# Kernel optimization log

Hardware: AMD Instinct MI355X
Metric: run time of the kernel (lower is better)

Reference implementation:

```python
import jax, jax.numpy as jnp
import numpy as np

V = 10000      # vocabulary_size
T = 20         # max_len
D = 512        # D_img == hidden size
H = 64         # actor/critic hidden
FI = 2048      # image feature dim
FB = 256       # box feature dim (FI + FB == 2304)
B = 1024       # batch
N_WORDS = 50   # allowed word_list size


def setup_inputs() -> dict:
    key = jax.random.key(0)
    ks = iter(jax.random.split(key, 40))
    def p(shape, s=0.02):
        return (jax.random.normal(next(ks), shape) * s).astype(jnp.float32)
    z = lambda *s: jnp.zeros(s, jnp.float32)
    inp = {
        "image_feature": jax.random.normal(next(ks), (B, FI), dtype=jnp.float32),
        "box_feature": jax.random.normal(next(ks), (B, FB), dtype=jnp.float32),
        # feature_resizer Linear(2304, D)
        "fr_w": p((FI + FB, D)), "fr_b": z(D),
        # _block dense1 / dense2 (each: Linear(D,D), GELU, Linear(D,D))
        "d1a_w": p((D, D)), "d1a_b": z(D), "d1b_w": p((D, D)), "d1b_b": z(D),
        "d2a_w": p((D, D)), "d2a_b": z(D), "d2b_w": p((D, D)), "d2b_b": z(D),
        # encoder LayerNorm (affine) + Linear(D, 512)
        "ln_g": jnp.ones((D,), jnp.float32), "ln_b": z(D),
        "eo_w": p((D, 512)), "eo_b": z(512),
        # word embedding
        "emb": p((V, 512)),
        # GRUCell weights, torch gate order (r, z, n)
        "gwi": p((512, 3 * 512)), "gwh": p((512, 3 * 512)),
        "gbi": z(3 * 512), "gbh": z(3 * 512),
        # actor: 512->64 tanh 64->64 tanh 64->V
        "a1_w": p((512, H)), "a1_b": z(H),
        "a2_w": p((H, H)), "a2_b": z(H),
        "a3_w": p((H, V), 0.01), "a3_b": z(V),
        # critic: 512->64 tanh 64->64 tanh 64->1
        "c1_w": p((512, H)), "c1_b": z(H),
        "c2_w": p((H, H)), "c2_b": z(H),
        "c3_w": p((H, 1)), "c3_b": z(1),
        # frozen word mask: 0 for allowed words, -1000 otherwise
        "word_mask": jnp.where(jnp.arange(V) < N_WORDS, 0.0, -1000.0).astype(jnp.float32),
    }
    return inp


def _ln(x, g=None, b=None):
    m = x.mean(-1, keepdims=True)
    v = x.var(-1, keepdims=True)
    y = (x - m) * jax.lax.rsqrt(v + 1e-5)
    return y if g is None else y * g + b


def _forward(image_feature, box_feature, fr_w, fr_b,
             d1a_w, d1a_b, d1b_w, d1b_b, d2a_w, d2a_b, d2b_w, d2b_b,
             ln_g, ln_b, eo_w, eo_b, emb, gwi, gwh, gbi, gbh,
             a1_w, a1_b, a2_w, a2_b, a3_w, a3_b,
             c1_w, c1_b, c2_w, c2_b, c3_w, c3_b, word_mask):
    gelu = lambda t: jax.nn.gelu(t, approximate=False)
    # feature resizer + residual block + LN + projection (encoder)
    x0 = jnp.concatenate([image_feature, box_feature], axis=1) @ fr_w + fr_b
    y = gelu(_ln(x0) @ d1a_w + d1a_b) @ d1b_w + d1b_b
    y = _ln(y + x0)
    x = x0 + (gelu(y @ d2a_w + d2a_b) @ d2b_w + d2b_b)
    img = _ln(x, ln_g, ln_b) @ eo_w + eo_b          # [B, 512]

    samp_key = jax.random.key(1)

    def step(carry, t):
        hx, ix = carry
        # torch: hx = GRUCell(input=hx, hidden=ix)
        gi = hx @ gwi + gbi
        gh = ix @ gwh + gbh
        gir, giz, gin = jnp.split(gi, 3, axis=-1)
        ghr, ghz, ghn = jnp.split(gh, 3, axis=-1)
        r = jax.nn.sigmoid(gir + ghr)
        zg = jax.nn.sigmoid(giz + ghz)
        n = jnp.tanh(gin + r * ghn)
        h = (1.0 - zg) * n + zg * ix                # new hidden [B, 512]
        logits = jnp.tanh(jnp.tanh(h @ a1_w + a1_b) @ a2_w + a2_b) @ a3_w + a3_b + word_mask
        logp = jax.nn.log_softmax(logits, axis=-1)  # [B, V]
        act = jax.random.categorical(jax.random.fold_in(samp_key, t), logp, axis=-1)  # [B]
        lp = jnp.take_along_axis(logp, act[:, None], axis=-1)[:, 0]
        ent = -jnp.sum(jnp.exp(logp) * logp, axis=-1)
        val = (jnp.tanh(jnp.tanh(h @ c1_w + c1_b) @ c2_w + c2_b) @ c3_w + c3_b)[:, 0]
        return (h, emb[act]), (act, lp, ent, val)

    _, (acts, lps, ents, vals) = jax.lax.scan(step, (img, jnp.zeros_like(img)), jnp.arange(T))
    # scan stacks along time first -> transpose to [B, T]
    return acts.T, lps.T, ents.T, vals.T[..., None]


def reference(image_feature, box_feature, fr_w, fr_b,
              d1a_w, d1a_b, d1b_w, d1b_b, d2a_w, d2a_b, d2b_w, d2b_b,
              ln_g, ln_b, eo_w, eo_b, emb, gwi, gwh, gbi, gbh,
              a1_w, a1_b, a2_w, a2_b, a3_w, a3_b,
              c1_w, c1_b, c2_w, c2_b, c3_w, c3_b, word_mask):
    return _forward(image_feature, box_feature, fr_w, fr_b,
                    d1a_w, d1a_b, d1b_w, d1b_b, d2a_w, d2a_b, d2b_w, d2b_b,
                    ln_g, ln_b, eo_w, eo_b, emb, gwi, gwh, gbi, gbh,
                    a1_w, a1_b, a2_w, a2_b, a3_w, a3_b,
                    c1_w, c1_b, c2_w, c2_b, c3_w, c3_b, word_mask)
```

## Files before the change

### kernel.cpp

```cpp
#include <hip/hip_runtime.h>
#include <math.h>
#include <stdint.h>

#define BB 1024
#define DD 512
#define VV 10000
#define TT 20
#define NW 50

__host__ __device__ __forceinline__ void tf2x32(uint32_t k0, uint32_t k1,
                                                uint32_t x0, uint32_t x1,
                                                uint32_t& o0, uint32_t& o1) {
  uint32_t ks2 = k0 ^ k1 ^ 0x1BD11BDAu;
  x0 += k0; x1 += k1;
#define ROTL(x,r) (((x)<<(r))|((x)>>(32-(r))))
#define RND(r) { x0 += x1; x1 = ROTL(x1,(r)); x1 ^= x0; }
  RND(13) RND(15) RND(26) RND(6)   x0 += k1;  x1 += ks2 + 1u;
  RND(17) RND(29) RND(16) RND(24)  x0 += ks2; x1 += k0 + 2u;
  RND(13) RND(15) RND(26) RND(6)   x0 += k0;  x1 += k1 + 3u;
  RND(17) RND(29) RND(16) RND(24)  x0 += k1;  x1 += ks2 + 4u;
  RND(13) RND(15) RND(26) RND(6)   x0 += ks2; x1 += k0 + 5u;
#undef RND
#undef ROTL
  o0 = x0; o1 = x1;
}

__device__ __forceinline__ float wave_sum(float v) {
#pragma unroll
  for (int o = 32; o > 0; o >>= 1) v += __shfl_xor(v, o, 64);
  return v;
}
__device__ __forceinline__ float wave_max(float v) {
#pragma unroll
  for (int o = 32; o > 0; o >>= 1) v = fmaxf(v, __shfl_xor(v, o, 64));
  return v;
}

__device__ __forceinline__ float gelu_f(float x) {
  float u = x / 1.4142135623730951f;
  float e = (float)erf((double)u);
  return x * (e + 1.0f) * 0.5f;
}

template<int MR, int ACT, bool RES, bool CONCAT>
__global__ __launch_bounds__(64) void wgemm_k(
    const float* __restrict__ A, const float* __restrict__ A2, int K1,
    const float* __restrict__ W, int ldw, const float* __restrict__ bias,
    const float* __restrict__ res, float* __restrict__ C, int N, int K)
{
  constexpr int TM = MR * 8;
  constexpr int ASTR = (TM == 64) ? 72 : 40;
  constexpr int WSTR = 40;
  constexpr int PA_N = (TM == 64) ? 16 : 8;
  __shared__ alignas(16) float As[64][ASTR];
  __shared__ alignas(16) float Ws[64][WSTR];
  const int bm = blockIdx.x * TM;
  const int bn = blockIdx.y * 32;
  const int lane = threadIdx.x;
  const int tr = (lane >> 3) * MR;
  const int tc = (lane & 7) << 2;
  const int arow = (TM == 64) ? lane : (lane & 31);
  const int akb  = (TM == 64) ? 0 : ((lane >> 5) * 32);
  const int wr0 = lane >> 3;
  const int wc  = (lane & 7) << 2;

  float4 pa[PA_N], pw[8];
  auto load_tile = [&](int k0) {
#pragma unroll
    for (int h = 0; h < PA_N; h++) {
      int gk = k0 + akb + 4 * h;
      if (CONCAT) {
        pa[h] = (gk < K1) ? *(const float4*)&A[(size_t)(bm + arow) * K1 + gk]
                          : *(const float4*)&A2[(size_t)(bm + arow) * (K - K1) + (gk - K1)];
      } else {
        pa[h] = *(const float4*)&A[(size_t)(bm + arow) * K + gk];
      }
    }
#pragma unroll
    for (int h = 0; h < 8; h++) {
      pw[h] = *(const float4*)&W[(size_t)(k0 + wr0 + 8 * h) * ldw + bn + wc];
    }
  };

  float acc[MR][4];
#pragma unroll
  for (int i = 0; i < MR; i++)
#pragma unroll
    for (int j = 0; j < 4; j++) acc[i][j] = 0.f;

  load_tile(0);
  for (int k0 = 0; k0 < K; k0 += 64) {
#pragma unroll
    for (int h = 0; h < PA_N; h++) {
      int kb = akb + 4 * h;
      As[kb + 0][arow] = pa[h].x; As[kb + 1][arow] = pa[h].y;
      As[kb + 2][arow] = pa[h].z; As[kb + 3][arow] = pa[h].w;
    }
#pragma unroll
    for (int h = 0; h < 8; h++) *(float4*)&Ws[wr0 + 8 * h][wc] = pw[h];
    if (k0 + 64 < K) load_tile(k0 + 64);
#pragma unroll
    for (int kk = 0; kk < 64; kk++) {
      float4 bv = *(const float4*)&Ws[kk][tc];
#pragma unroll
      for (int ih = 0; ih < MR / 4; ih++) {
        float4 av = *(const float4*)&As[kk][tr + 4 * ih];
        float* ap = (float*)&av;
#pragma unroll
        for (int q = 0; q < 4; q++) {
          int i = 4 * ih + q;
          acc[i][0] = fmaf(ap[q], bv.x, acc[i][0]);
          acc[i][1] = fmaf(ap[q], bv.y, acc[i][1]);
          acc[i][2] = fmaf(ap[q], bv.z, acc[i][2]);
          acc[i][3] = fmaf(ap[q], bv.w, acc[i][3]);
        }
      }
    }
  }
#pragma unroll
  for (int i = 0; i < MR; i++) {
    int m = bm + tr + i;
    float4 o;
    float* op = (float*)&o;
#pragma unroll
    for (int j = 0; j < 4; j++) {
      int n = bn + tc + j;
      float v = acc[i][j] + bias[n];
      if (ACT == 1) v = gelu_f(v);
      if (RES) v = v + res[(size_t)m * N + n];
      op[j] = v;
    }
    *(float4*)&C[(size_t)m * N + bn + tc] = o;
  }
}

template<bool AFFINE, bool ADD>
__global__ __launch_bounds__(256) void lnorm_k(
    const float* __restrict__ X, const float* __restrict__ X2,
    const float* __restrict__ g, const float* __restrict__ bt,
    float* __restrict__ Y)
{
  __shared__ float red[8];
  int row = blockIdx.x, tid = threadIdx.x;
  const float* x = X + (size_t)row * DD;
  float v0 = x[tid], v1 = x[tid + 256];
  if (ADD) {
    const float* x2 = X2 + (size_t)row * DD;
    v0 += x2[tid]; v1 += x2[tid + 256];
  }
  float s = wave_sum(v0 + v1);
  if ((tid & 63) == 0) red[tid >> 6] = s;
  __syncthreads();
  float mean = (red[0] + red[1] + red[2] + red[3]) * (1.0f / 512.0f);
  float d0 = v0 - mean, d1 = v1 - mean;
  float s2 = wave_sum(d0 * d0 + d1 * d1);
  if ((tid & 63) == 0) red[4 + (tid >> 6)] = s2;
  __syncthreads();
  float var = (red[4] + red[5] + red[6] + red[7]) * (1.0f / 512.0f);
  float rs = (float)(1.0 / sqrt((double)(var + 1e-5f)));
  float y0 = d0 * rs, y1 = d1 * rs;
  if (AFFINE) {
    y0 = y0 * g[tid] + bt[tid];
    y1 = y1 * g[tid + 256] + bt[tid + 256];
  }
  Y[(size_t)row * DD + tid] = y0;
  Y[(size_t)row * DD + tid + 256] = y1;
}

__global__ __launch_bounds__(256) void gru_head(
    const float* __restrict__ gi, const float* __restrict__ table,
    const float* __restrict__ gbh, const float* __restrict__ emb,
    const float* __restrict__ a1w, const float* __restrict__ a1b,
    const float* __restrict__ a2w, const float* __restrict__ a2b,
    const float* __restrict__ a3w, const float* __restrict__ a3b,
    const float* __restrict__ c1w, const float* __restrict__ c1b,
    const float* __restrict__ c2w, const float* __restrict__ c2b,
    const float* __restrict__ c3w, const float* __restrict__ c3b,
    const float* __restrict__ wmask,
    float* __restrict__ hx, float* __restrict__ out,
    int t, uint32_t fk0, uint32_t fk1)
{
  int w = threadIdx.x >> 6;
  int lane = threadIdx.x & 63;
  int b = blockIdx.x * 4 + w;
  __shared__ float sh[4][DD];
  __shared__ float st1[4][64], st2[4][64], sc1[4][64];

  int a = (t > 0) ? (int)out[(size_t)b * TT + (t - 1)] : -1;
  const float* ghb = (a >= 0) ? (table + (size_t)a * 1536) : gbh;
  const float* gib = gi + (size_t)b * 1536;
  const float* er  = (a >= 0) ? (emb + (size_t)a * DD) : nullptr;
#pragma unroll
  for (int jj = 0; jj < 8; jj++) {
    int j = lane + 64 * jj;
    float ixv = (a >= 0) ? er[j] : 0.f;
    float r = (float)(1.0 / (1.0 + exp(-(double)(gib[j] + ghb[j]))));
    float z = (float)(1.0 / (1.0 + exp(-(double)(gib[DD + j] + ghb[DD + j]))));
    float narg = gib[2 * DD + j] + r * ghb[2 * DD + j];
    float n = (float)tanh((double)narg);
    float h = (1.0f - z) * n + z * ixv;
    sh[w][j] = h;
    hx[(size_t)b * DD + j] = h;
  }
  __syncthreads();

  float aa0 = 0, aa1 = 0, aa2 = 0, aa3 = 0, ca0 = 0, ca1 = 0, ca2 = 0, ca3 = 0;
  for (int k = 0; k < DD; k += 4) {
    float h0 = sh[w][k], h1 = sh[w][k + 1], h2 = sh[w][k + 2], h3 = sh[w][k + 3];
    aa0 = fmaf(h0, a1w[(k + 0) * 64 + lane], aa0);
    aa1 = fmaf(h1, a1w[(k + 1) * 64 + lane], aa1);
    aa2 = fmaf(h2, a1w[(k + 2) * 64 + lane], aa2);
    aa3 = fmaf(h3, a1w[(k + 3) * 64 + lane], aa3);
    ca0 = fmaf(h0, c1w[(k + 0) * 64 + lane], ca0);
    ca1 = fmaf(h1, c1w[(k + 1) * 64 + lane], ca1);
    ca2 = fmaf(h2, c1w[(k + 2) * 64 + lane], ca2);
    ca3 = fmaf(h3, c1w[(k + 3) * 64 + lane], ca3);
  }
  st1[w][lane] = (float)tanh((double)(((aa0 + aa1) + (aa2 + aa3)) + a1b[lane]));
  sc1[w][lane] = (float)tanh((double)(((ca0 + ca1) + (ca2 + ca3)) + c1b[lane]));
  __syncthreads();

  float a2acc = 0, c2acc = 0;
  for (int k = 0; k < 64; k++) {
    a2acc = fmaf(st1[w][k], a2w[k * 64 + lane], a2acc);
    c2acc = fmaf(sc1[w][k], c2w[k * 64 + lane], c2acc);
  }
  st2[w][lane] = (float)tanh((double)(a2acc + a2b[lane]));
  float t2c = (float)tanh((double)(c2acc + c2b[lane]));
  __syncthreads();

  float val = wave_sum(t2c * c3w[lane]) + c3b[0];

  float lg = -INFINITY;
  if (lane < NW) {
    float s = 0;
    for (int k = 0; k < 64; k++) s = fmaf(st2[w][k], a3w[k * VV + lane], s);
    lg = (s + a3b[lane]) + wmask[lane];
  }

  float m = wave_max(lg);
  float shf = 0.f, e = 0.f;
  if (lane < NW) { shf = lg - m; e = (float)exp((double)shf); }
  float se = wave_sum(e);
  float lse = (float)log((double)se);
  float logp = shf - lse;
  float term = 0.f;
  if (lane < NW) { float p = (float)exp((double)logp); term = p * logp; }
  float ent = -wave_sum(term);

  float score = -INFINITY;
  if (lane < NW) {
    uint32_t i = (uint32_t)b * (uint32_t)VV + (uint32_t)lane;
    uint32_t o0, o1;
    tf2x32(fk0, fk1, 0u, i, o0, o1);
    uint32_t bits = o0 ^ o1;
    uint32_t mant = bits >> 9;
    float u = (mant == 0u) ? 1.17549435e-38f
                           : (float)mant * 1.1920928955078125e-7f;
    float l1 = (float)log((double)u);
    float l2 = (float)log((double)(-l1));
    score = -l2 + logp;
  }

  float best = score; int bi = lane;
#pragma unroll
  for (int off = 32; off > 0; off >>= 1) {
    float ob = __shfl_xor(best, off, 64);
    int oi = __shfl_xor(bi, off, 64);
    if (ob > best || (ob == best && oi < bi)) { best = ob; bi = oi; }
  }
  float lp = __shfl(logp, bi, 64);

  if (lane == 0) {
    out[(size_t)b * TT + t] = (float)bi;
    out[(size_t)BB * TT + (size_t)b * TT + t] = lp;
    out[2 * (size_t)BB * TT + (size_t)b * TT + t] = ent;
    out[3 * (size_t)BB * TT + (size_t)b * TT + t] = val;
  }
}

__global__ __launch_bounds__(256) void diag_k(float* out, float code, int n) {
  int i = blockIdx.x * 256 + threadIdx.x;
  if (i < n) out[i] = code;
}

extern "C" void kernel_launch(void* const* d_in, const int* in_sizes, int n_in,
                              void* d_out, int out_size, void* d_ws, size_t ws_size,
                              hipStream_t stream) {
  static const int EXP_SIZES[34] = {
    2097152, 262144, 1179648, 512, 262144, 512, 262144, 512, 262144, 512,
    262144, 512, 512, 512, 262144, 512, 5120000, 786432, 786432, 1536,
    1536, 32768, 64, 4096, 64, 640000, 10000, 32768, 64, 4096,
    64, 64, 1, 10000 };
  double code = 0.0;
  if (n_in != 34) code = 1e6 + (double)n_in;
  else {
    for (int i = 0; i < 34; i++)
      if (in_sizes[i] != EXP_SIZES[i]) { code = 2e6 + i * 1e4 + (in_sizes[i] % 10000); break; }
  }
  if (code == 0.0 && out_size != 4 * BB * TT) code = 3e6 + (double)(out_size % 1000000);
  if (code == 0.0 && ws_size < (size_t)24 * 1024 * 1024) {
    size_t kb = ws_size / 1024; if (kb > 999999) kb = 999999;
    code = 4e6 + (double)kb;
  }
  if (code != 0.0) {
    diag_k<<<(out_size + 255) / 256, 256, 0, stream>>>((float*)d_out, (float)code, out_size);
    return;
  }

  const float* image = (const float*)d_in[0];
  const float* boxf  = (const float*)d_in[1];
  const float* fr_w  = (const float*)d_in[2];
  const float* fr_b  = (const float*)d_in[3];
  const float* d1a_w = (const float*)d_in[4];
  const float* d1a_b = (const float*)d_in[5];
  const float* d1b_w = (const float*)d_in[6];
  const float* d1b_b = (const float*)d_in[7];
  const float* d2a_w = (const float*)d_in[8];
  const float* d2a_b = (const float*)d_in[9];
  const float* d2b_w = (const float*)d_in[10];
  const float* d2b_b = (const float*)d_in[11];
  const float* ln_g  = (const float*)d_in[12];
  const float* ln_b  = (const float*)d_in[13];
  const float* eo_w  = (const float*)d_in[14];
  const float* eo_b  = (const float*)d_in[15];
  const float* emb   = (const float*)d_in[16];
  const float* gwi   = (const float*)d_in[17];
  const float* gwh   = (const float*)d_in[18];
  const float* gbi   = (const float*)d_in[19];
  const float* gbh   = (const float*)d_in[20];
  const float* a1w   = (const float*)d_in[21];
  const float* a1b   = (const float*)d_in[22];
  const float* a2w   = (const float*)d_in[23];
  const float* a2b   = (const float*)d_in[24];
  const float* a3w   = (const float*)d_in[25];
  const float* a3b   = (const float*)d_in[26];
  const float* c1w   = (const float*)d_in[27];
  const float* c1b   = (const float*)d_in[28];
  const float* c2w   = (const float*)d_in[29];
  const float* c2b   = (const float*)d_in[30];
  const float* c3w   = (const float*)d_in[31];
  const float* c3b   = (const float*)d_in[32];
  const float* wmask = (const float*)d_in[33];

  float* ws = (float*)d_ws;
  const size_t R = (size_t)BB * DD;
  float* hx    = ws;
  float* gi    = ws + R;
  float* Q     = ws + 4 * R;
  float* S     = ws + 5 * R;
  float* U     = ws + 6 * R;
  float* table = ws + 7 * R;
  float* P     = gi;
  float* out = (float*)d_out;

  dim3 wblk(64);
  wgemm_k<4, 0, false, false><<<dim3(2, 48), wblk, 0, stream>>>(emb, nullptr, 0, gwh, 1536, gbh, nullptr, table, 1536, 512);
  wgemm_k<4, 0, false, true><<<dim3(32, 16), wblk, 0, stream>>>(image, boxf, 2048, fr_w, 512, fr_b, nullptr, P, 512, 2304);
  lnorm_k<false, false><<<BB, dim3(256), 0, stream>>>(P, nullptr, nullptr, nullptr, Q);
  wgemm_k<4, 1, false, false><<<dim3(32, 16), wblk, 0, stream>>>(Q, nullptr, 0, d1a_w, 512, d1a_b, nullptr, S, 512, 512);
  wgemm_k<4, 0, false, false><<<dim3(32, 16), wblk, 0, stream>>>(S, nullptr, 0, d1b_w, 512, d1b_b, nullptr, U, 512, 512);
  lnorm_k<false, true><<<BB, dim3(256), 0, stream>>>(U, P, nullptr, nullptr, Q);
  wgemm_k<4, 1, false, false><<<dim3(32, 16), wblk, 0, stream>>>(Q, nullptr, 0, d2a_w, 512, d2a_b, nullptr, S, 512, 512);
  wgemm_k<4, 0, true, false><<<dim3(32, 16), wblk, 0, stream>>>(S, nullptr, 0, d2b_w, 512, d2b_b, P, U, 512, 512);
  lnorm_k<true, false><<<BB, dim3(256), 0, stream>>>(U, nullptr, ln_g, ln_b, Q);
  wgemm_k<4, 0, false, false><<<dim3(32, 16), wblk, 0, stream>>>(Q, nullptr, 0, eo_w, 512, eo_b, nullptr, hx, 512, 512);

  for (int t = 0; t < TT; t++) {
    uint32_t fk0, fk1;
    tf2x32(0u, 1u, 0u, (uint32_t)t, fk0, fk1);
    wgemm_k<8, 0, false, false><<<dim3(16, 48), wblk, 0, stream>>>(hx, nullptr, 0, gwi, 1536, gbi, nullptr, gi, 1536, 512);
    gru_head<<<dim3(BB / 4), dim3(256), 0, stream>>>(gi, table, gbh, emb,
                                      a1w, a1b, a2w, a2b, a3w, a3b,
                                      c1w, c1b, c2w, c2b, c3w, c3b,
                                      wmask, hx, out, t, fk0, fk1);
  }
}
```

Measured before the change: 1.824 ms.

## Replace LDS-tiled GEMM with a simple per-column register-blocked GEMM

Swaps the shared-memory tiled GEMM for a kernel where each thread owns one output column and accumulates 8 rows in registers. The weight values are read straight from global memory with coalesced loads, and the activation rows are read with wave-uniform addresses that can become broadcast or scalar loads. This removes the LDS staging, the transposed stores and their synchronisation, and launches many more small blocks. In exchange it gives up reuse of weights across rows: every row-block streams the whole weight strip through the caches, which raises L2 traffic and makes the kernel more sensitive to memory latency.

```diff
diff --git a/kernel.cpp b/kernel.cpp
--- a/kernel.cpp
+++ b/kernel.cpp
@@ -42,95 +42,47 @@
   return x * (e + 1.0f) * 0.5f;
 }
 
-template<int MR, int ACT, bool RES, bool CONCAT>
-__global__ __launch_bounds__(64) void wgemm_k(
+template<int M, int ACT, bool RES, bool CONCAT>
+__global__ __launch_bounds__(64) void sbgemm_k(
     const float* __restrict__ A, const float* __restrict__ A2, int K1,
-    const float* __restrict__ W, int ldw, const float* __restrict__ bias,
+    const float* __restrict__ W, const float* __restrict__ bias,
     const float* __restrict__ res, float* __restrict__ C, int N, int K)
 {
-  constexpr int TM = MR * 8;
-  constexpr int ASTR = (TM == 64) ? 72 : 40;
-  constexpr int WSTR = 40;
-  constexpr int PA_N = (TM == 64) ? 16 : 8;
-  __shared__ alignas(16) float As[64][ASTR];
-  __shared__ alignas(16) float Ws[64][WSTR];
-  const int bm = blockIdx.x * TM;
-  const int bn = blockIdx.y * 32;
-  const int lane = threadIdx.x;
-  const int tr = (lane >> 3) * MR;
-  const int tc = (lane & 7) << 2;
-  const int arow = (TM == 64) ? lane : (lane & 31);
-  const int akb  = (TM == 64) ? 0 : ((lane >> 5) * 32);
-  const int wr0 = lane >> 3;
-  const int wc  = (lane & 7) << 2;
-
-  float4 pa[PA_N], pw[8];
-  auto load_tile = [&](int k0) {
-#pragma unroll
-    for (int h = 0; h < PA_N; h++) {
-      int gk = k0 + akb + 4 * h;
+  const int m0 = blockIdx.x * M;
+  const int n = blockIdx.y * 64 + threadIdx.x;
+  const float* wp = W + n;
+  float acc[M];
+#pragma unroll
+  for (int m = 0; m < M; m++) acc[m] = 0.f;
+
+#pragma unroll 4
+  for (int k = 0; k < K; k += 4) {
+    float w0 = wp[(size_t)(k + 0) * N];
+    float w1 = wp[(size_t)(k + 1) * N];
+    float w2 = wp[(size_t)(k + 2) * N];
+    float w3 = wp[(size_t)(k + 3) * N];
+#pragma unroll
+    for (int m = 0; m < M; m++) {
+      const float* ar;
       if (CONCAT) {
-        pa[h] = (gk < K1) ? *(const float4*)&A[(size_t)(bm + arow) * K1 + gk]
-                          : *(const float4*)&A2[(size_t)(bm + arow) * (K - K1) + (gk - K1)];
+        ar = (k < K1) ? &A[(size_t)(m0 + m) * K1 + k]
+                      : &A2[(size_t)(m0 + m) * (K - K1) + (k - K1)];
       } else {
-        pa[h] = *(const float4*)&A[(size_t)(bm + arow) * K + gk];
+        ar = &A[(size_t)(m0 + m) * K + k];
       }
+      float a0 = ar[0], a1 = ar[1], a2 = ar[2], a3 = ar[3];
+      acc[m] = fmaf(a0, w0, acc[m]);
+      acc[m] = fmaf(a1, w1, acc[m]);
+      acc[m] = fmaf(a2, w2, acc[m]);
+      acc[m] = fmaf(a3, w3, acc[m]);
     }
-#pragma unroll
-    for (int h = 0; h < 8; h++) {
-      pw[h] = *(const float4*)&W[(size_t)(k0 + wr0 + 8 * h) * ldw + bn + wc];
-    }
-  };
-
-  float acc[MR][4];
-#pragma unroll
-  for (int i = 0; i < MR; i++)
-#pragma unroll
-    for (int j = 0; j < 4; j++) acc[i][j] = 0.f;
-
-  load_tile(0);
-  for (int k0 = 0; k0 < K; k0 += 64) {
-#pragma unroll
-    for (int h = 0; h < PA_N; h++) {
-      int kb = akb + 4 * h;
-      As[kb + 0][arow] = pa[h].x; As[kb + 1][arow] = pa[h].y;
-      As[kb + 2][arow] = pa[h].z; As[kb + 3][arow] = pa[h].w;
-    }
-#pragma unroll
-    for (int h = 0; h < 8; h++) *(float4*)&Ws[wr0 + 8 * h][wc] = pw[h];
-    if (k0 + 64 < K) load_tile(k0 + 64);
-#pragma unroll
-    for (int kk = 0; kk < 64; kk++) {
-      float4 bv = *(const float4*)&Ws[kk][tc];
-#pragma unroll
-      for (int ih = 0; ih < MR / 4; ih++) {
-        float4 av = *(const float4*)&As[kk][tr + 4 * ih];
-        float* ap = (float*)&av;
-#pragma unroll
-        for (int q = 0; q < 4; q++) {
-          int i = 4 * ih + q;
-          acc[i][0] = fmaf(ap[q], bv.x, acc[i][0]);
-          acc[i][1] = fmaf(ap[q], bv.y, acc[i][1]);
-          acc[i][2] = fmaf(ap[q], bv.z, acc[i][2]);
-          acc[i][3] = fmaf(ap[q], bv.w, acc[i][3]);
-        }
-      }
-    }
-  }
-#pragma unroll
-  for (int i = 0; i < MR; i++) {
-    int m = bm + tr + i;
-    float4 o;
-    float* op = (float*)&o;
-#pragma unroll
-    for (int j = 0; j < 4; j++) {
-      int n = bn + tc + j;
-      float v = acc[i][j] + bias[n];
-      if (ACT == 1) v = gelu_f(v);
-      if (RES) v = v + res[(size_t)m * N + n];
-      op[j] = v;
-    }
-    *(float4*)&C[(size_t)m * N + bn + tc] = o;
+  }
+#pragma unroll
+  for (int m = 0; m < M; m++) {
+    float v = acc[m] + bias[n];
+    if (ACT == 1) v = gelu_f(v);
+    if (RES) v = v + res[(size_t)(m0 + m) * N + n];
+    C[(size_t)(m0 + m) * N + n] = v;
   }
 }
 
@@ -355,21 +307,21 @@
   float* out = (float*)d_out;
 
   dim3 wblk(64);
-  wgemm_k<4, 0, false, false><<<dim3(2, 48), wblk, 0, stream>>>(emb, nullptr, 0, gwh, 1536, gbh, nullptr, table, 1536, 512);
-  wgemm_k<4, 0, false, true><<<dim3(32, 16), wblk, 0, stream>>>(image, boxf, 2048, fr_w, 512, fr_b, nullptr, P, 512, 2304);
+  sbgemm_k<8, 0, false, false><<<dim3(8, 24), wblk, 0, stream>>>(emb, nullptr, 0, gwh, gbh, nullptr, table, 1536, 512);
+  sbgemm_k<8, 0, false, true><<<dim3(128, 8), wblk, 0, stream>>>(image, boxf, 2048, fr_w, fr_b, nullptr, P, 512, 2304);
   lnorm_k<false, false><<<BB, dim3(256), 0, stream>>>(P, nullptr, nullptr, nullptr, Q);
-  wgemm_k<4, 1, false, false><<<dim3(32, 16), wblk, 0, stream>>>(Q, nullptr, 0, d1a_w, 512, d1a_b, nullptr, S, 512, 512);
-  wgemm_k<4, 0, false, false><<<dim3(32, 16), wblk, 0, stream>>>(S, nullptr, 0, d1b_w, 512, d1b_b, nullptr, U, 512, 512);
+  sbgemm_k<8, 1, false, false><<<dim3(128, 8), wblk, 0, stream>>>(Q, nullptr, 0, d1a_w, d1a_b, nullptr, S, 512, 512);
+  sbgemm_k<8, 0, false, false><<<dim3(128, 8), wblk, 0, stream>>>(S, nullptr, 0, d1b_w, d1b_b, nullptr, U, 512, 512);
   lnorm_k<false, true><<<BB, dim3(256), 0, stream>>>(U, P, nullptr, nullptr, Q);
-  wgemm_k<4, 1, false, false><<<dim3(32, 16), wblk, 0, stream>>>(Q, nullptr, 0, d2a_w, 512, d2a_b, nullptr, S, 512, 512);
-  wgemm_k<4, 0, true, false><<<dim3(32, 16), wblk, 0, stream>>>(S, nullptr, 0, d2b_w, 512, d2b_b, P, U, 512, 512);
+  sbgemm_k<8, 1, false, false><<<dim3(128, 8), wblk, 0, stream>>>(Q, nullptr, 0, d2a_w, d2a_b, nullptr, S, 512, 512);
+  sbgemm_k<8, 0, true, false><<<dim3(128, 8), wblk, 0, stream>>>(S, nullptr, 0, d2b_w, d2b_b, P, U, 512, 512);
   lnorm_k<true, false><<<BB, dim3(256), 0, stream>>>(U, nullptr, ln_g, ln_b, Q);
-  wgemm_k<4, 0, false, false><<<dim3(32, 16), wblk, 0, stream>>>(Q, nullptr, 0, eo_w, 512, eo_b, nullptr, hx, 512, 512);
+  sbgemm_k<8, 0, false, false><<<dim3(128, 8), wblk, 0, stream>>>(Q, nullptr, 0, eo_w, eo_b, nullptr, hx, 512, 512);
 
   for (int t = 0; t < TT; t++) {
     uint32_t fk0, fk1;
     tf2x32(0u, 1u, 0u, (uint32_t)t, fk0, fk1);
-    wgemm_k<8, 0, false, false><<<dim3(16, 48), wblk, 0, stream>>>(hx, nullptr, 0, gwi, 1536, gbi, nullptr, gi, 1536, 512);
+    sbgemm_k<8, 0, false, false><<<dim3(128, 24), wblk, 0, stream>>>(hx, nullptr, 0, gwi, gbi, nullptr, gi, 1536, 512);
     gru_head<<<dim3(BB / 4), dim3(256), 0, stream>>>(gi, table, gbh, emb,
                                       a1w, a1b, a2w, a2b, a3w, a3b,
                                       c1w, c1b, c2w, c2b, c3w, c3b,
```

New measurement: 2.640 ms. 1.45x slower.

## Replace single-wave GEMM with 256-thread double-buffered tiled GEMM

Applied to the files above, without the earlier changes.

The 64-thread wgemm kernel is replaced by a 256-thread tgemm kernel with 64-wide N tiles, 32-deep K steps and double-buffered shared memory for A and W. Global loads for the next K slice are issued while the current slice is computed, with one barrier per step. The aim is better occupancy, more reuse of each W tile, and latency hiding in the per-step GRU input GEMM and the encoder GEMMs. Grid sizes are adjusted to match. The cost is fewer outputs per thread in the TM=32 variant, which lowers register reuse and adds block-level sync.

```diff
diff --git a/kernel.cpp b/kernel.cpp
--- a/kernel.cpp
+++ b/kernel.cpp
@@ -42,33 +42,32 @@
   return x * (e + 1.0f) * 0.5f;
 }
 
-template<int MR, int ACT, bool RES, bool CONCAT>
-__global__ __launch_bounds__(64) void wgemm_k(
+template<int TM, int ACT, bool RES, bool CONCAT>
+__global__ __launch_bounds__(256) void tgemm_k(
     const float* __restrict__ A, const float* __restrict__ A2, int K1,
     const float* __restrict__ W, int ldw, const float* __restrict__ bias,
     const float* __restrict__ res, float* __restrict__ C, int N, int K)
 {
-  constexpr int TM = MR * 8;
-  constexpr int ASTR = (TM == 64) ? 72 : 40;
-  constexpr int WSTR = 40;
-  constexpr int PA_N = (TM == 64) ? 16 : 8;
-  __shared__ alignas(16) float As[64][ASTR];
-  __shared__ alignas(16) float Ws[64][WSTR];
+  constexpr int MR   = TM / 16;
+  constexpr int ASTR = TM + 4;
+  constexpr int NA   = TM / 32;
+  __shared__ alignas(16) float As[2][32][ASTR];
+  __shared__ alignas(16) float Ws[2][32][68];
   const int bm = blockIdx.x * TM;
-  const int bn = blockIdx.y * 32;
-  const int lane = threadIdx.x;
-  const int tr = (lane >> 3) * MR;
-  const int tc = (lane & 7) << 2;
-  const int arow = (TM == 64) ? lane : (lane & 31);
-  const int akb  = (TM == 64) ? 0 : ((lane >> 5) * 32);
-  const int wr0 = lane >> 3;
-  const int wc  = (lane & 7) << 2;
-
-  float4 pa[PA_N], pw[8];
+  const int bn = blockIdx.y * 64;
+  const int t  = threadIdx.x;
+  const int tr = (t >> 4) * MR;
+  const int tc = (t & 15) << 2;
+  const int arow = t & (TM - 1);
+  const int akb  = (TM == 64) ? ((t >> 6) << 3) : ((t >> 5) << 2);
+  const int wr   = t >> 3;
+  const int wc   = (t & 7) << 3;
+
+  float4 pa[NA], pw0, pw1;
   auto load_tile = [&](int k0) {
 #pragma unroll
-    for (int h = 0; h < PA_N; h++) {
-      int gk = k0 + akb + 4 * h;
+    for (int h = 0; h < NA; h++) {
+      int gk = k0 + akb + ((TM == 64) ? 4 * h : 0);
       if (CONCAT) {
         pa[h] = (gk < K1) ? *(const float4*)&A[(size_t)(bm + arow) * K1 + gk]
                           : *(const float4*)&A2[(size_t)(bm + arow) * (K - K1) + (gk - K1)];
@@ -76,11 +75,20 @@
         pa[h] = *(const float4*)&A[(size_t)(bm + arow) * K + gk];
       }
     }
-#pragma unroll
-    for (int h = 0; h < 8; h++) {
-      pw[h] = *(const float4*)&W[(size_t)(k0 + wr0 + 8 * h) * ldw + bn + wc];
-    }
+    const float* wsrc = &W[(size_t)(k0 + wr) * ldw + bn + wc];
+    pw0 = *(const float4*)(wsrc);
+    pw1 = *(const float4*)(wsrc + 4);
   };
+  auto store_tile = [&](int buf) {
+#pragma unroll
+    for (int h = 0; h < NA; h++) {
+      int kb = akb + ((TM == 64) ? 4 * h : 0);
+      As[buf][kb + 0][arow] = pa[h].x; As[buf][kb + 1][arow] = pa[h].y;
+      As[buf][kb + 2][arow] = pa[h].z; As[buf][kb + 3][arow] = pa[h].w;
+    }
+    *(float4*)&Ws[buf][wr][wc]     = pw0;
+    *(float4*)&Ws[buf][wr][wc + 4] = pw1;
+  };
 
   float acc[MR][4];
 #pragma unroll
@@ -89,32 +97,40 @@
     for (int j = 0; j < 4; j++) acc[i][j] = 0.f;
 
   load_tile(0);
-  for (int k0 = 0; k0 < K; k0 += 64) {
-#pragma unroll
-    for (int h = 0; h < PA_N; h++) {
-      int kb = akb + 4 * h;
-      As[kb + 0][arow] = pa[h].x; As[kb + 1][arow] = pa[h].y;
-      As[kb + 2][arow] = pa[h].z; As[kb + 3][arow] = pa[h].w;
-    }
-#pragma unroll
-    for (int h = 0; h < 8; h++) *(float4*)&Ws[wr0 + 8 * h][wc] = pw[h];
-    if (k0 + 64 < K) load_tile(k0 + 64);
-#pragma unroll
-    for (int kk = 0; kk < 64; kk++) {
-      float4 bv = *(const float4*)&Ws[kk][tc];
-#pragma unroll
-      for (int ih = 0; ih < MR / 4; ih++) {
-        float4 av = *(const float4*)&As[kk][tr + 4 * ih];
-        float* ap = (float*)&av;
+  store_tile(0);
+  __syncthreads();
+  const int NT = K / 32;
+  for (int it = 0; it < NT; it++) {
+    const int cur = it & 1;
+    if (it + 1 < NT) load_tile(32 * (it + 1));
+#pragma unroll
+    for (int kk = 0; kk < 32; kk++) {
+      float4 bv = *(const float4*)&Ws[cur][kk][tc];
+      if (TM == 64) {
+        float4 av = *(const float4*)&As[cur][kk][tr];
+        const float* ap = (const float*)&av;
 #pragma unroll
         for (int q = 0; q < 4; q++) {
-          int i = 4 * ih + q;
-          acc[i][0] = fmaf(ap[q], bv.x, acc[i][0]);
-          acc[i][1] = fmaf(ap[q], bv.y, acc[i][1]);
-          acc[i][2] = fmaf(ap[q], bv.z, acc[i][2]);
-          acc[i][3] = fmaf(ap[q], bv.w, acc[i][3]);
+          acc[q][0] = fmaf(ap[q], bv.x, acc[q][0]);
+          acc[q][1] = fmaf(ap[q], bv.y, acc[q][1]);
+          acc[q][2] = fmaf(ap[q], bv.z, acc[q][2]);
+          acc[q][3] = fmaf(ap[q], bv.w, acc[q][3]);
         }
+      } else {
+        float2 av = *(const float2*)&As[cur][kk][tr];
+        acc[0][0] = fmaf(av.x, bv.x, acc[0][0]);
+        acc[0][1] = fmaf(av.x, bv.y, acc[0][1]);
+        acc[0][2] = fmaf(av.x, bv.z, acc[0][2]);
+        acc[0][3] = fmaf(av.x, bv.w, acc[0][3]);
+        acc[1][0] = fmaf(av.y, bv.x, acc[1][0]);
+        acc[1][1] = fmaf(av.y, bv.y, acc[1][1]);
+        acc[1][2] = fmaf(av.y, bv.z, acc[1][2]);
+        acc[1][3] = fmaf(av.y, bv.w, acc[1][3]);
       }
+    }
+    if (it + 1 < NT) {
+      store_tile(cur ^ 1);
+      __syncthreads();
     }
   }
 #pragma unroll
@@ -354,23 +370,23 @@
   float* P     = gi;
   float* out = (float*)d_out;
 
-  dim3 wblk(64);
-  wgemm_k<4, 0, false, false><<<dim3(2, 48), wblk, 0, stream>>>(emb, nullptr, 0, gwh, 1536, gbh, nullptr, table, 1536, 512);
-  wgemm_k<4, 0, false, true><<<dim3(32, 16), wblk, 0, stream>>>(image, boxf, 2048, fr_w, 512, fr_b, nullptr, P, 512, 2304);
-  lnorm_k<false, false><<<BB, dim3(256), 0, stream>>>(P, nullptr, nullptr, nullptr, Q);
-  wgemm_k<4, 1, false, false><<<dim3(32, 16), wblk, 0, stream>>>(Q, nullptr, 0, d1a_w, 512, d1a_b, nullptr, S, 512, 512);
-  wgemm_k<4, 0, false, false><<<dim3(32, 16), wblk, 0, stream>>>(S, nullptr, 0, d1b_w, 512, d1b_b, nullptr, U, 512, 512);
-  lnorm_k<false, true><<<BB, dim3(256), 0, stream>>>(U, P, nullptr, nullptr, Q);
-  wgemm_k<4, 1, false, false><<<dim3(32, 16), wblk, 0, stream>>>(Q, nullptr, 0, d2a_w, 512, d2a_b, nullptr, S, 512, 512);
-  wgemm_k<4, 0, true, false><<<dim3(32, 16), wblk, 0, stream>>>(S, nullptr, 0, d2b_w, 512, d2b_b, P, U, 512, 512);
-  lnorm_k<true, false><<<BB, dim3(256), 0, stream>>>(U, nullptr, ln_g, ln_b, Q);
-  wgemm_k<4, 0, false, false><<<dim3(32, 16), wblk, 0, stream>>>(Q, nullptr, 0, eo_w, 512, eo_b, nullptr, hx, 512, 512);
+  dim3 blk(256);
+  tgemm_k<64, 0, false, false><<<dim3(1, 24), blk, 0, stream>>>(emb, nullptr, 0, gwh, 1536, gbh, nullptr, table, 1536, 512);
+  tgemm_k<32, 0, false, true><<<dim3(32, 8), blk, 0, stream>>>(image, boxf, 2048, fr_w, 512, fr_b, nullptr, P, 512, 2304);
+  lnorm_k<false, false><<<BB, blk, 0, stream>>>(P, nullptr, nullptr, nullptr, Q);
+  tgemm_k<32, 1, false, false><<<dim3(32, 8), blk, 0, stream>>>(Q, nullptr, 0, d1a_w, 512, d1a_b, nullptr, S, 512, 512);
+  tgemm_k<32, 0, false, false><<<dim3(32, 8), blk, 0, stream>>>(S, nullptr, 0, d1b_w, 512, d1b_b, nullptr, U, 512, 512);
+  lnorm_k<false, true><<<BB, blk, 0, stream>>>(U, P, nullptr, nullptr, Q);
+  tgemm_k<32, 1, false, false><<<dim3(32, 8), blk, 0, stream>>>(Q, nullptr, 0, d2a_w, 512, d2a_b, nullptr, S, 512, 512);
+  tgemm_k<32, 0, true, false><<<dim3(32, 8), blk, 0, stream>>>(S, nullptr, 0, d2b_w, 512, d2b_b, P, U, 512, 512);
+  lnorm_k<true, false><<<BB, blk, 0, stream>>>(U, nullptr, ln_g, ln_b, Q);
+  tgemm_k<32, 0, false, false><<<dim3(32, 8), blk, 0, stream>>>(Q, nullptr, 0, eo_w, 512, eo_b, nullptr, hx, 512, 512);
 
   for (int t = 0; t < TT; t++) {
     uint32_t fk0, fk1;
     tf2x32(0u, 1u, 0u, (uint32_t)t, fk0, fk1);
-    wgemm_k<8, 0, false, false><<<dim3(16, 48), wblk, 0, stream>>>(hx, nullptr, 0, gwi, 1536, gbi, nullptr, gi, 1536, 512);
-    gru_head<<<dim3(BB / 4), dim3(256), 0, stream>>>(gi, table, gbh, emb,
+    tgemm_k<64, 0, false, false><<<dim3(16, 24), blk, 0, stream>>>(hx, nullptr, 0, gwi, 1536, gbi, nullptr, gi, 1536, 512);
+    gru_head<<<dim3(BB / 4), blk, 0, stream>>>(gi, table, gbh, emb,
                                       a1w, a1b, a2w, a2b, a3w, a3b,
                                       c1w, c1b, c2w, c2b, c3w, c3b,
                                       wmask, hx, out, t, fk0, fk1);
```

New measurement: 1.790 ms. No clear change (-1.9%).
